# Kernel tuning notes

Measured on AMD Instinct MI355X. Metric: run time of the kernel, lower is better.

Reference implementation:

```python
import jax, jax.numpy as jnp
import numpy as np

IN_FEATURES = 2048
OUT_FEATURES = 2048
BATCH = 4096


def setup_inputs() -> dict:
    key = jax.random.key(0)
    k1, k2, k3, k4 = jax.random.split(key, 4)
    bound = 1.0 / (IN_FEATURES ** 0.5)
    x_re = jax.random.normal(k1, (BATCH, IN_FEATURES), dtype=jnp.float32)
    x_im = jax.random.normal(k2, (BATCH, IN_FEATURES), dtype=jnp.float32)
    # filters: (out_features, in_features), re/im each uniform(-bound, bound)
    w_re = jax.random.uniform(k3, (OUT_FEATURES, IN_FEATURES), dtype=jnp.float32, minval=-bound, maxval=bound)
    w_im = jax.random.uniform(k4, (OUT_FEATURES, IN_FEATURES), dtype=jnp.float32, minval=-bound, maxval=bound)
    return {"x_re": x_re, "x_im": x_im, "w_re": w_re, "w_im": w_im}


def reference(x_re, x_im, w_re, w_im):
    # Complex linear: (x_re + i x_im) @ (w_re + i w_im)^T, expressed as 4 real GEMMs.
    # Equivalent to torch: (inputs.unsqueeze(1) * filters).sum(-1) with complex64.
    out_re = jnp.einsum('bi,oi->bo', x_re, w_re) - jnp.einsum('bi,oi->bo', x_im, w_im)
    out_im = jnp.einsum('bi,oi->bo', x_re, w_im) + jnp.einsum('bi,oi->bo', x_im, w_re)
    # stack re/im -> (2, batch, out) to keep a single real-dtype output
    return jnp.stack([out_re, out_im], axis=0)
```

## Files before the change

kernel.cpp:

```cpp
#include <hip/hip_runtime.h>

typedef __bf16 bf16_t;
typedef __bf16 bf16x8 __attribute__((ext_vector_type(8)));
typedef __bf16 bf16x4 __attribute__((ext_vector_type(4)));
typedef float f32x4 __attribute__((ext_vector_type(4)));

#define M_DIM 4096
#define N_DIM 4096
#define K_DIM 4096
#define OUTF 2048
#define INF 2048
#define LDK 4096
#define NT 64

__global__ __launch_bounds__(256) void pack_ab(
    const float* __restrict__ xre, const float* __restrict__ xim,
    const float* __restrict__ wre, const float* __restrict__ wim,
    bf16_t* __restrict__ Abf, bf16_t* __restrict__ Bbf)
{
  size_t gid = (size_t)blockIdx.x * 256 + threadIdx.x;
  size_t e8  = gid * 8;
  const size_t MAT = (size_t)4096 * 4096;
  bool isB = e8 >= MAT;
  size_t e = isB ? (e8 - MAT) : e8;
  int row = (int)(e >> 12);
  int k   = (int)(e & 4095);

  const float* src;
  float s = 1.0f;
  if (!isB) {
    src = (k < INF) ? (xre + (size_t)row * INF + k)
                    : (xim + (size_t)row * INF + (k - INF));
  } else {
    if (row < OUTF) {
      if (k < INF) { src = wre + (size_t)row * INF + k; }
      else         { src = wim + (size_t)row * INF + (k - INF); s = -1.0f; }
    } else {
      int o = row - OUTF;
      src = (k < INF) ? (wim + (size_t)o * INF + k)
                      : (wre + (size_t)o * INF + (k - INF));
    }
  }
  const float4* p = reinterpret_cast<const float4*>(src);
  float4 f0 = p[0];
  float4 f1 = p[1];
  bf16x8 v;
  v[0] = (bf16_t)(f0.x * s); v[1] = (bf16_t)(f0.y * s);
  v[2] = (bf16_t)(f0.z * s); v[3] = (bf16_t)(f0.w * s);
  v[4] = (bf16_t)(f1.x * s); v[5] = (bf16_t)(f1.y * s);
  v[6] = (bf16_t)(f1.z * s); v[7] = (bf16_t)(f1.w * s);
  bf16_t* dst = (isB ? Bbf : Abf) + e;
  *reinterpret_cast<bf16x8*>(dst) = v;
}

__device__ __forceinline__ void gld_lds16(const void* g, void* l) {
  __builtin_amdgcn_global_load_lds(
      (const __attribute__((address_space(1))) void*)g,
      (__attribute__((address_space(3))) void*)l,
      16, 0, 0);
}


template<int QM, int QN>
__device__ __forceinline__ void mfma_quad(f32x4 (&acc)[8][4],
                                          const bf16x8 (&aF)[4][2],
                                          const bf16x8 (&bF)[2][2]) {
  __builtin_amdgcn_s_setprio(1);
#pragma unroll
  for (int m = 0; m < 4; ++m)
#pragma unroll
    for (int n = 0; n < 2; ++n) {
      f32x4 v = acc[QM * 4 + m][QN * 2 + n];
      v = __builtin_amdgcn_mfma_f32_16x16x32_bf16(aF[m][0], bF[n][0], v, 0, 0, 0);
      v = __builtin_amdgcn_mfma_f32_16x16x32_bf16(aF[m][1], bF[n][1], v, 0, 0, 0);
      acc[QM * 4 + m][QN * 2 + n] = v;
    }
  __builtin_amdgcn_s_setprio(0);
}

__global__ __launch_bounds__(512, 2) void gemm256(
    const bf16_t* __restrict__ A, const bf16_t* __restrict__ B,
    float* __restrict__ out)
{
  __shared__ alignas(16) bf16_t lds[2 * 32768];
  char* Lb = (char*)lds;

  const int tid  = threadIdx.x;
  const int lane = tid & 63;
  const int wid  = tid >> 6;
  const int wm   = wid >> 2;
  const int wn   = wid & 3;
  const int lr   = lane & 15;
  const int kg   = (lane >> 4) * 16;
  const int xm   = ((lr & 3) << 4) | (((lr >> 2) & 1) << 6);

  int bid = blockIdx.x;
  int swz = (bid & 7) * 32 + (bid >> 3);
  const int bm = swz >> 4;
  const int bn = swz & 15;

  int rS[2], kS[2];
#pragma unroll
  for (int j = 0; j < 2; ++j) {
    int P   = j * 8192 + tid * 16;
    int row = P >> 7;
    int p   = P & 127;
    int L   = p ^ ((row & 3) << 4) ^ (((row >> 2) & 1) << 6);
    rS[j] = row;
    kS[j] = L >> 1;
  }
  const bf16_t* As0 = A + (size_t)(bm * 256 + rS[0]) * LDK + kS[0];
  const bf16_t* As1 = A + (size_t)(bm * 256 + rS[1]) * LDK + kS[1];
  const bf16_t* Bs0 = B + (size_t)(bn * 256 + rS[0]) * LDK + kS[0];
  const bf16_t* Bs1 = B + (size_t)(bn * 256 + rS[1]) * LDK + kS[1];
  const int dst16 = tid * 16;

#define STAGE_A(t, h, c) do {                                                  \
    gld_lds16(As0 + (size_t)(h) * 128 * LDK + (t) * 64,                        \
              Lb + (c) * 65536 + (h) * 16384 + dst16);                         \
    gld_lds16(As1 + (size_t)(h) * 128 * LDK + (t) * 64,                        \
              Lb + (c) * 65536 + (h) * 16384 + 8192 + dst16);                  \
  } while (0)
#define STAGE_B(t, h, c) do {                                                  \
    gld_lds16(Bs0 + (size_t)(h) * 128 * LDK + (t) * 64,                        \
              Lb + (c) * 65536 + 32768 + (h) * 16384 + dst16);                 \
    gld_lds16(Bs1 + (size_t)(h) * 128 * LDK + (t) * 64,                        \
              Lb + (c) * 65536 + 32768 + (h) * 16384 + 8192 + dst16);          \
  } while (0)
#define RD_A(c, qm, m, ks)                                                     \
  (*(const bf16x8*)(Lb + (c) * 65536 + wm * 16384 +                            \
                    ((qm) * 64 + (m) * 16 + lr) * 128 +                        \
                    ((((ks) * 64) | kg) ^ xm)))
#define RD_B(c, qn, n, ks)                                                     \
  (*(const bf16x8*)(Lb + (c) * 65536 + 32768 + (wn >> 1) * 16384 +             \
                    ((wn & 1) * 64 + (qn) * 32 + (n) * 16 + lr) * 128 +        \
                    ((((ks) * 64) | kg) ^ xm)))
#define BAR()   __builtin_amdgcn_s_barrier()
#define SB()    __builtin_amdgcn_sched_barrier(0)
#define ISSUE_Q1(c) do {                                                       \
    _Pragma("unroll")                                                          \
    for (int m_ = 0; m_ < 4; ++m_) {                                           \
      a0[m_][0] = RD_A(c, 0, m_, 0);                                           \
      a0[m_][1] = RD_A(c, 0, m_, 1);                                           \
    }                                                                          \
    _Pragma("unroll")                                                          \
    for (int n_ = 0; n_ < 2; ++n_) {                                           \
      b0[n_][0] = RD_B(c, 0, n_, 0);                                           \
      b0[n_][1] = RD_B(c, 0, n_, 1);                                           \
    }                                                                          \
  } while (0)

  f32x4 acc[8][4];
#pragma unroll
  for (int i = 0; i < 8; ++i)
#pragma unroll
    for (int j = 0; j < 4; ++j)
      acc[i][j] = (f32x4){0.f, 0.f, 0.f, 0.f};

  bf16x8 a0[4][2], b0[2][2];

  STAGE_A(0, 0, 0); STAGE_A(0, 1, 0);
  STAGE_B(0, 0, 0); STAGE_B(0, 1, 0);
  STAGE_A(1, 0, 1);
  asm volatile("s_waitcnt vmcnt(2)" ::: "memory");
  BAR();
  ISSUE_Q1(0);
  SB();

  for (int t = 0; t < NT; ++t) {
    const int c = t & 1;
    bf16x8 a1[4][2], b1[2][2];

    if (t + 1 < NT) STAGE_A(t + 1, 1, c ^ 1);
#pragma unroll
    for (int n = 0; n < 2; ++n) {
      b1[n][0] = RD_B(c, 1, n, 0);
      b1[n][1] = RD_B(c, 1, n, 1);
    }
    SB();
    asm volatile("s_waitcnt lgkmcnt(4)" ::: "memory");
    SB();
    mfma_quad<0, 0>(acc, a0, b0);

    if (t + 1 < NT) STAGE_B(t + 1, 0, c ^ 1);
#pragma unroll
    for (int m = 0; m < 4; ++m) {
      a1[m][0] = RD_A(c, 1, m, 0);
      a1[m][1] = RD_A(c, 1, m, 1);
    }
    SB();
    asm volatile("s_waitcnt lgkmcnt(8)" ::: "memory");
    SB();
    mfma_quad<0, 1>(acc, a0, b1);

    if (t + 1 < NT) STAGE_B(t + 1, 1, c ^ 1);
    asm volatile("s_waitcnt lgkmcnt(0)" ::: "memory");
    SB();
    mfma_quad<1, 1>(acc, a1, b1);
    BAR();

    if (t + 2 < NT) STAGE_A(t + 2, 0, c);
    if (t + 2 < NT) {
      asm volatile("s_waitcnt vmcnt(2)" ::: "memory");
    } else if (t + 1 < NT) {
      asm volatile("s_waitcnt vmcnt(0)" ::: "memory");
    }
    BAR();
    mfma_quad<1, 0>(acc, a1, b0);
    if (t + 1 < NT) {
      SB();
      ISSUE_Q1(c ^ 1);
      SB();
    }
  }

  const size_t imOff = (size_t)M_DIM * OUTF;
  const int fq = (lane >> 4) * 4;
  const bool isIm = (bn * 256) >= OUTF;
  float* obase = out + (isIm ? imOff : 0);
  const int colBase = bn * 256 - (isIm ? OUTF : 0) + wn * 64;
#pragma unroll
  for (int ar = 0; ar < 8; ++ar) {
    int gr = bm * 256 + wm * 128 + ar * 16 + fq;
#pragma unroll
    for (int cc = 0; cc < 4; ++cc) {
      int gc = colBase + cc * 16 + lr;
#pragma unroll
      for (int j = 0; j < 4; ++j)
        obase[(size_t)(gr + j) * OUTF + gc] = acc[ar][cc][j];
    }
  }
#undef STAGE_A
#undef STAGE_B
#undef RD_A
#undef RD_B
#undef BAR
#undef SB
#undef ISSUE_Q1
}

__global__ __launch_bounds__(256) void gemm_fused(
    const float* __restrict__ xre, const float* __restrict__ xim,
    const float* __restrict__ wre, const float* __restrict__ wim,
    float* __restrict__ out)
{
  __shared__ alignas(16) bf16_t As[128 * 40];
  __shared__ alignas(16) bf16_t Bs[128 * 40];

  int tid = threadIdx.x;
  int bid = blockIdx.x;
  int swz = (bid & 7) * 128 + (bid >> 3);
  int bm = swz >> 5;
  int bn = swz & 31;

  int lane = tid & 63;
  int w    = tid >> 6;
  int wm   = (w >> 1) * 64;
  int wn   = (w & 1) * 64;
  int lr   = lane & 15;
  int lk   = (lane >> 4) * 8;

  f32x4 acc[4][4];
#pragma unroll
  for (int m = 0; m < 4; ++m)
#pragma unroll
    for (int n = 0; n < 4; ++n)
      acc[m][n] = (f32x4){0.f, 0.f, 0.f, 0.f};

  int srow = tid >> 3;
  int scol = (tid & 7) * 4;

  bool nIm  = (bn * 128) >= OUTF;
  int nbase = nIm ? (bn * 128 - OUTF) : (bn * 128);

  for (int kt = 0; kt < K_DIM / 32; ++kt) {
    int k0 = kt * 32;
    bool kHi = (k0 >= INF);
    int kk = kHi ? (k0 - INF) : k0;

    const float* Asrc = (kHi ? xim : xre) + (size_t)(bm * 128) * INF + kk;
    const float* Bsrc;
    float s = 1.0f;
    if (!nIm) { if (!kHi) { Bsrc = wre; } else { Bsrc = wim; s = -1.0f; } }
    else      { Bsrc = kHi ? wre : wim; }
    Bsrc += (size_t)nbase * INF + kk;

    float4 av[4], bv[4];
#pragma unroll
    for (int i = 0; i < 4; ++i) {
      av[i] = *reinterpret_cast<const float4*>(Asrc + (size_t)(srow + i * 32) * INF + scol);
      bv[i] = *reinterpret_cast<const float4*>(Bsrc + (size_t)(srow + i * 32) * INF + scol);
    }
    __syncthreads();
#pragma unroll
    for (int i = 0; i < 4; ++i) {
      bf16x4 a4, b4;
      a4[0] = (bf16_t)av[i].x; a4[1] = (bf16_t)av[i].y;
      a4[2] = (bf16_t)av[i].z; a4[3] = (bf16_t)av[i].w;
      b4[0] = (bf16_t)(bv[i].x * s); b4[1] = (bf16_t)(bv[i].y * s);
      b4[2] = (bf16_t)(bv[i].z * s); b4[3] = (bf16_t)(bv[i].w * s);
      *reinterpret_cast<bf16x4*>(&As[(srow + i * 32) * 40 + scol]) = a4;
      *reinterpret_cast<bf16x4*>(&Bs[(srow + i * 32) * 40 + scol]) = b4;
    }
    __syncthreads();

    bf16x8 a[4], b[4];
#pragma unroll
    for (int m = 0; m < 4; ++m)
      a[m] = *reinterpret_cast<const bf16x8*>(&As[(wm + m * 16 + lr) * 40 + lk]);
#pragma unroll
    for (int n = 0; n < 4; ++n)
      b[n] = *reinterpret_cast<const bf16x8*>(&Bs[(wn + n * 16 + lr) * 40 + lk]);
#pragma unroll
    for (int m = 0; m < 4; ++m)
#pragma unroll
      for (int n = 0; n < 4; ++n)
        acc[m][n] = __builtin_amdgcn_mfma_f32_16x16x32_bf16(a[m], b[n], acc[m][n], 0, 0, 0);
  }
  __syncthreads();

  const size_t imOff = (size_t)M_DIM * OUTF;
  int fq = (lane >> 4) * 4;
#pragma unroll
  for (int m = 0; m < 4; ++m) {
    int gr = bm * 128 + wm + m * 16 + fq;
#pragma unroll
    for (int n = 0; n < 4; ++n) {
      int gc = bn * 128 + wn + n * 16 + lr;
      float* dst = (gc < OUTF) ? (out + (size_t)gr * OUTF + gc)
                               : (out + imOff + (size_t)gr * OUTF + (gc - OUTF));
#pragma unroll
      for (int j = 0; j < 4; ++j)
        dst[(size_t)j * OUTF] = acc[m][n][j];
    }
  }
}

extern "C" void kernel_launch(void* const* d_in, const int* in_sizes, int n_in,
                              void* d_out, int out_size, void* d_ws, size_t ws_size,
                              hipStream_t stream) {
  const float* xre = (const float*)d_in[0];
  const float* xim = (const float*)d_in[1];
  const float* wre = (const float*)d_in[2];
  const float* wim = (const float*)d_in[3];
  float* out = (float*)d_out;

  const size_t need = (size_t)2 * 4096 * 4096 * sizeof(bf16_t);
  if (ws_size >= need) {
    bf16_t* Abf = (bf16_t*)d_ws;
    bf16_t* Bbf = Abf + (size_t)4096 * 4096;
    hipLaunchKernelGGL(pack_ab, dim3(16384), dim3(256), 0, stream,
                       xre, xim, wre, wim, Abf, Bbf);
    hipLaunchKernelGGL(gemm256, dim3(256), dim3(512), 0, stream,
                       Abf, Bbf, out);
  } else {
    hipLaunchKernelGGL(gemm_fused, dim3(1024), dim3(256), 0, stream,
                       xre, xim, wre, wim, out);
  }
}
```

Measured before the change: 141.9 us.

## Restructure GEMM main loop into barrier-synchronized 8-phase ping-pong schedule

Rewrites the bf16 MFMA main loop from a software-pipelined single-iteration body with sched_barriers and partial lgkmcnt waits into an explicitly unrolled two-tile loop. Each quadrant of MFMAs is bracketed by workgroup barriers and full LDS waits, and the global-to-LDS staging order changes so that B is prefetched before A. The aim is a ping-pong style schedule where waves alternate between memory and compute phases. In exchange it adds many more barriers per K-step and removes the overlap of LDS reads with the in-flight MFMAs, which could serialize work.

Result: slower. 145.2 us (+2.3%).

```diff
diff --git a/kernel.cpp b/kernel.cpp
--- a/kernel.cpp
+++ b/kernel.cpp
@@ -135,18 +135,29 @@
   (*(const bf16x8*)(Lb + (c) * 65536 + 32768 + (wn >> 1) * 16384 +             \
                     ((wn & 1) * 64 + (qn) * 32 + (n) * 16 + lr) * 128 +        \
                     ((((ks) * 64) | kg) ^ xm)))
-#define BAR()   __builtin_amdgcn_s_barrier()
-#define SB()    __builtin_amdgcn_sched_barrier(0)
-#define ISSUE_Q1(c) do {                                                       \
+#define BAR()     __builtin_amdgcn_s_barrier()
+#define LGKM(N)   asm volatile("s_waitcnt lgkmcnt(" #N ")" ::: "memory")
+#define VMC(N)    asm volatile("s_waitcnt vmcnt(" #N ")" ::: "memory")
+#define RD12(c) do {                                                           \
     _Pragma("unroll")                                                          \
     for (int m_ = 0; m_ < 4; ++m_) {                                           \
-      a0[m_][0] = RD_A(c, 0, m_, 0);                                           \
-      a0[m_][1] = RD_A(c, 0, m_, 1);                                           \
+      a0[m_][0] = RD_A(c, 0, m_, 0); a0[m_][1] = RD_A(c, 0, m_, 1);            \
     }                                                                          \
     _Pragma("unroll")                                                          \
     for (int n_ = 0; n_ < 2; ++n_) {                                           \
-      b0[n_][0] = RD_B(c, 0, n_, 0);                                           \
-      b0[n_][1] = RD_B(c, 0, n_, 1);                                           \
+      b0[n_][0] = RD_B(c, 0, n_, 0); b0[n_][1] = RD_B(c, 0, n_, 1);            \
+    }                                                                          \
+  } while (0)
+#define RD4(c) do {                                                            \
+    _Pragma("unroll")                                                          \
+    for (int n_ = 0; n_ < 2; ++n_) {                                           \
+      b1[n_][0] = RD_B(c, 1, n_, 0); b1[n_][1] = RD_B(c, 1, n_, 1);            \
+    }                                                                          \
+  } while (0)
+#define RD8(c) do {                                                            \
+    _Pragma("unroll")                                                          \
+    for (int m_ = 0; m_ < 4; ++m_) {                                           \
+      a1[m_][0] = RD_A(c, 1, m_, 0); a1[m_][1] = RD_A(c, 1, m_, 1);            \
     }                                                                          \
   } while (0)
 
@@ -157,61 +168,67 @@
     for (int j = 0; j < 4; ++j)
       acc[i][j] = (f32x4){0.f, 0.f, 0.f, 0.f};
 
-  bf16x8 a0[4][2], b0[2][2];
-
   STAGE_A(0, 0, 0); STAGE_A(0, 1, 0);
   STAGE_B(0, 0, 0); STAGE_B(0, 1, 0);
-  STAGE_A(1, 0, 1);
-  asm volatile("s_waitcnt vmcnt(2)" ::: "memory");
+  STAGE_B(1, 0, 1); STAGE_B(1, 1, 1);
+  VMC(4);
   BAR();
-  ISSUE_Q1(0);
-  SB();
-
-  for (int t = 0; t < NT; ++t) {
-    const int c = t & 1;
-    bf16x8 a1[4][2], b1[2][2];
-
-    if (t + 1 < NT) STAGE_A(t + 1, 1, c ^ 1);
-#pragma unroll
-    for (int n = 0; n < 2; ++n) {
-      b1[n][0] = RD_B(c, 1, n, 0);
-      b1[n][1] = RD_B(c, 1, n, 1);
-    }
-    SB();
-    asm volatile("s_waitcnt lgkmcnt(4)" ::: "memory");
-    SB();
+
+  for (int i = 0; i < NT / 2; ++i) {
+    const int u  = 2 * i;
+    const bool s2 = (u + 2 < NT);
+    const bool s3 = (u + 3 < NT);
+    bf16x8 a0[4][2], a1[4][2], b0[2][2], b1[2][2];
+
+    RD12(0);
+    STAGE_A(u + 1, 0, 1);
+    LGKM(8);
+    BAR(); LGKM(0);
     mfma_quad<0, 0>(acc, a0, b0);
-
-    if (t + 1 < NT) STAGE_B(t + 1, 0, c ^ 1);
-#pragma unroll
-    for (int m = 0; m < 4; ++m) {
-      a1[m][0] = RD_A(c, 1, m, 0);
-      a1[m][1] = RD_A(c, 1, m, 1);
-    }
-    SB();
-    asm volatile("s_waitcnt lgkmcnt(8)" ::: "memory");
-    SB();
+    BAR();
+
+    RD4(0);
+    STAGE_A(u + 1, 1, 1);
+    BAR(); LGKM(0);
     mfma_quad<0, 1>(acc, a0, b1);
-
-    if (t + 1 < NT) STAGE_B(t + 1, 1, c ^ 1);
-    asm volatile("s_waitcnt lgkmcnt(0)" ::: "memory");
-    SB();
+    BAR();
+
+    RD8(0);
+    if (s2) STAGE_B(u + 2, 0, 0);
+    BAR(); LGKM(0);
     mfma_quad<1, 1>(acc, a1, b1);
     BAR();
 
-    if (t + 2 < NT) STAGE_A(t + 2, 0, c);
-    if (t + 2 < NT) {
-      asm volatile("s_waitcnt vmcnt(2)" ::: "memory");
-    } else if (t + 1 < NT) {
-      asm volatile("s_waitcnt vmcnt(0)" ::: "memory");
-    }
+    if (s2) STAGE_B(u + 2, 1, 0);
     BAR();
     mfma_quad<1, 0>(acc, a1, b0);
-    if (t + 1 < NT) {
-      SB();
-      ISSUE_Q1(c ^ 1);
-      SB();
-    }
+    if (s2) { VMC(4); } else { VMC(0); }
+    BAR();
+
+    RD12(1);
+    if (s2) STAGE_A(u + 2, 0, 0);
+    LGKM(8);
+    BAR(); LGKM(0);
+    mfma_quad<0, 0>(acc, a0, b0);
+    BAR();
+
+    RD4(1);
+    if (s2) STAGE_A(u + 2, 1, 0);
+    BAR(); LGKM(0);
+    mfma_quad<0, 1>(acc, a0, b1);
+    BAR();
+
+    RD8(1);
+    if (s3) STAGE_B(u + 3, 0, 1);
+    BAR(); LGKM(0);
+    mfma_quad<1, 1>(acc, a1, b1);
+    BAR();
+
+    if (s3) STAGE_B(u + 3, 1, 1);
+    BAR();
+    mfma_quad<1, 0>(acc, a1, b0);
+    if (s3) { VMC(4); } else { VMC(0); }
+    BAR();
   }
 
   const size_t imOff = (size_t)M_DIM * OUTF;
@@ -235,8 +252,11 @@
 #undef RD_A
 #undef RD_B
 #undef BAR
-#undef SB
-#undef ISSUE_Q1
+#undef LGKM
+#undef VMC
+#undef RD12
+#undef RD4
+#undef RD8
 }
 
 __global__ __launch_bounds__(256) void gemm_fused(
```

## Use 3-multiplication complex GEMM (Gauss trick) with new pack and fused kernel

Applied to the files above, without the earlier changes.

Replaces the 4-real-GEMM formulation, packed as one 4096x4096x4096 GEMM, with the Gauss 3M trick. It packs (xr+xi), xi, xr and wr, -(wr+wi), wi-wr into bf16, then runs three K=2048 products, sharing accumulators so the real and imaginary outputs are built from three partial sums. This cuts MFMA work by a quarter but changes the tile to 256x128 with more barriers per k-tile, and adds extra rounding from bf16 sums of operands. The pack now reads and writes a somewhat different volume of data.

After: 164.0 us. 1.16x slower.

```diff
diff --git a/kernel.cpp b/kernel.cpp
--- a/kernel.cpp
+++ b/kernel.cpp
@@ -6,12 +6,236 @@
 typedef float f32x4 __attribute__((ext_vector_type(4)));
 
 #define M_DIM 4096
-#define N_DIM 4096
-#define K_DIM 4096
 #define OUTF 2048
 #define INF 2048
 #define LDK 4096
 #define NT 64
+#define LDK2 2048
+#define NT3 96
+
+__device__ __forceinline__ float mfq(float x) { return x; }
+
+__global__ __launch_bounds__(256) void pack_3m(
+    const float* __restrict__ xre, const float* __restrict__ xim,
+    const float* __restrict__ wre, const float* __restrict__ wim,
+    bf16_t* __restrict__ ws)
+{
+  size_t e = ((size_t)blockIdx.x * 256 + threadIdx.x) * 8;
+  const size_t AB = 25165824;
+  bf16x8 v;
+  if (e < AB) {
+    int seg = (int)(e / 8388608);
+    size_t off = e - (size_t)seg * 8388608;
+    size_t base = (off >> 11) * (size_t)INF + (off & 2047);
+    const float4* pr = reinterpret_cast<const float4*>(xre + base);
+    const float4* pi = reinterpret_cast<const float4*>(xim + base);
+#pragma unroll
+    for (int h = 0; h < 2; ++h) {
+      float4 fr = pr[h], fi = pi[h];
+      float r[4] = {fr.x, fr.y, fr.z, fr.w};
+      float ii[4] = {fi.x, fi.y, fi.z, fi.w};
+#pragma unroll
+      for (int j = 0; j < 4; ++j) {
+        float o = (seg == 0) ? (r[j] + ii[j]) : ((seg == 1) ? ii[j] : r[j]);
+        v[h * 4 + j] = (bf16_t)o;
+      }
+    }
+  } else {
+    size_t eb = e - AB;
+    int seg = (int)(eb / 4194304);
+    size_t off = eb - (size_t)seg * 4194304;
+    size_t base = (off >> 11) * (size_t)INF + (off & 2047);
+    const float4* pr = reinterpret_cast<const float4*>(wre + base);
+    const float4* pi = reinterpret_cast<const float4*>(wim + base);
+#pragma unroll
+    for (int h = 0; h < 2; ++h) {
+      float4 fr = pr[h], fi = pi[h];
+      float r[4] = {fr.x, fr.y, fr.z, fr.w};
+      float ii[4] = {fi.x, fi.y, fi.z, fi.w};
+#pragma unroll
+      for (int j = 0; j < 4; ++j) {
+        float o = (seg == 0) ? r[j] : ((seg == 1) ? -(r[j] + ii[j]) : (ii[j] - r[j]));
+        v[h * 4 + j] = (bf16_t)o;
+      }
+    }
+  }
+  *reinterpret_cast<bf16x8*>(ws + e) = v;
+}
+
+__device__ __forceinline__ void gld_lds16(const void* g, void* l) {
+  __builtin_amdgcn_global_load_lds(
+      (const __attribute__((address_space(1))) void*)g,
+      (__attribute__((address_space(3))) void*)l,
+      16, 0, 0);
+}
+
+__global__ __launch_bounds__(512, 2) void gemm3m(
+    const bf16_t* __restrict__ ws, float* __restrict__ out)
+{
+  __shared__ alignas(16) bf16_t lds[2 * 24576];
+  char* Lb = (char*)lds;
+
+  const int tid  = threadIdx.x;
+  const int lane = tid & 63;
+  const int wid  = tid >> 6;
+  const int wm2  = wid >> 1;
+  const int wn2  = wid & 1;
+  const int lr   = lane & 15;
+  const int kg   = (lane >> 4) * 16;
+  const int xm   = ((lr & 3) << 4) | (((lr >> 2) & 1) << 6);
+
+  int bid = blockIdx.x;
+  int swz = (bid & 7) * 32 + (bid >> 3);
+  const int bm = swz >> 4;
+  const int bn = swz & 15;
+
+  const int rowbase = tid >> 3;
+  const int pby     = (tid & 7) * 16;
+  const int Lg      = pby ^ ((rowbase & 3) << 4) ^ (((rowbase >> 2) & 1) << 6);
+  const int kelem   = Lg >> 1;
+  const int dst16   = tid * 16;
+
+  const bf16_t* Sb  = ws;
+  const bf16_t* XIb = ws + 8388608;
+  const bf16_t* XRb = ws + 16777216;
+  const bf16_t* B1b = ws + 25165824;
+  const bf16_t* B2b = ws + 29360128;
+  const bf16_t* B3b = ws + 33554432;
+
+  const size_t aoff = (size_t)(bm * 256 + rowbase) * LDK2 + kelem;
+  const size_t boff = (size_t)(bn * 128 + rowbase) * LDK2 + kelem;
+  const bf16_t* aB[3] = {Sb + aoff, XIb + aoff, XRb + aoff};
+  const bf16_t* bB[3] = {B1b + boff, B2b + boff, B3b + boff};
+
+#define STAGE_AH(u, h, c) do {                                                 \
+    int p_ = (u) >> 5, lt_ = (u) & 31;                                         \
+    const bf16_t* ab_ = aB[0];                                                 \
+    if (p_ == 1) ab_ = aB[1]; else if (p_ == 2) ab_ = aB[2];                   \
+    _Pragma("unroll")                                                          \
+    for (int j_ = 0; j_ < 2; ++j_)                                             \
+      gld_lds16(ab_ + (size_t)((h) * 128 + j_ * 64) * LDK2 + lt_ * 64,         \
+                Lb + (c) * 49152 + (h) * 16384 + j_ * 8192 + dst16);           \
+  } while (0)
+#define STAGE_B3(u, c) do {                                                    \
+    int p_ = (u) >> 5, lt_ = (u) & 31;                                         \
+    const bf16_t* bb_ = bB[0];                                                 \
+    if (p_ == 1) bb_ = bB[1]; else if (p_ == 2) bb_ = bB[2];                   \
+    _Pragma("unroll")                                                          \
+    for (int j_ = 0; j_ < 2; ++j_)                                             \
+      gld_lds16(bb_ + (size_t)(j_ * 64) * LDK2 + lt_ * 64,                     \
+                Lb + (c) * 49152 + 32768 + j_ * 8192 + dst16);                 \
+  } while (0)
+#define RD_A3(c, h, m_, ks)                                                    \
+  (*(const bf16x8*)(Lb + (c) * 49152 +                                         \
+      (wm2 * 64 + (h) * 32 + (m_) * 16 + lr) * 128 + ((((ks) * 64) | kg) ^ xm)))
+#define RD_B3(c, g, n_, ks)                                                    \
+  (*(const bf16x8*)(Lb + (c) * 49152 + 32768 +                                 \
+      (wn2 * 64 + (g) * 32 + (n_) * 16 + lr) * 128 + ((((ks) * 64) | kg) ^ xm)))
+#define BAR()   __builtin_amdgcn_s_barrier()
+#define LGKM0() asm volatile("s_waitcnt lgkmcnt(0)" ::: "memory")
+#define MQ(ACC, h, g, AF, BF) do {                                             \
+    __builtin_amdgcn_s_setprio(1);                                             \
+    _Pragma("unroll")                                                          \
+    for (int m_ = 0; m_ < 2; ++m_)                                             \
+    _Pragma("unroll")                                                          \
+    for (int n_ = 0; n_ < 2; ++n_) {                                           \
+      f32x4 v_ = ACC[(h) * 2 + m_][(g) * 2 + n_];                              \
+      v_ = __builtin_amdgcn_mfma_f32_16x16x32_bf16(AF[m_][0], BF[n_][0], v_,   \
+                                                   0, 0, 0);                   \
+      v_ = __builtin_amdgcn_mfma_f32_16x16x32_bf16(AF[m_][1], BF[n_][1], v_,   \
+                                                   0, 0, 0);                   \
+      ACC[(h) * 2 + m_][(g) * 2 + n_] = v_;                                    \
+    }                                                                          \
+    __builtin_amdgcn_s_setprio(0);                                             \
+  } while (0)
+#define KTILE(u, ACC) do {                                                     \
+    const int c_ = (u) & 1;                                                    \
+    bf16x8 a0[2][2], a1[2][2], b0[2][2], b1[2][2];                             \
+    _Pragma("unroll")                                                          \
+    for (int m_ = 0; m_ < 2; ++m_) {                                           \
+      a0[m_][0] = RD_A3(c_, 0, m_, 0); a0[m_][1] = RD_A3(c_, 0, m_, 1);        \
+    }                                                                          \
+    _Pragma("unroll")                                                          \
+    for (int n_ = 0; n_ < 2; ++n_) {                                           \
+      b0[n_][0] = RD_B3(c_, 0, n_, 0); b0[n_][1] = RD_B3(c_, 0, n_, 1);        \
+    }                                                                          \
+    if ((u) + 1 < NT3) STAGE_AH((u) + 1, 1, c_ ^ 1);                           \
+    BAR(); LGKM0();                                                            \
+    MQ(ACC, 0, 0, a0, b0);                                                     \
+    BAR();                                                                     \
+    _Pragma("unroll")                                                          \
+    for (int n_ = 0; n_ < 2; ++n_) {                                           \
+      b1[n_][0] = RD_B3(c_, 1, n_, 0); b1[n_][1] = RD_B3(c_, 1, n_, 1);        \
+    }                                                                          \
+    if ((u) + 1 < NT3) STAGE_B3((u) + 1, c_ ^ 1);                              \
+    BAR(); LGKM0();                                                            \
+    MQ(ACC, 0, 1, a0, b1);                                                     \
+    BAR();                                                                     \
+    _Pragma("unroll")                                                          \
+    for (int m_ = 0; m_ < 2; ++m_) {                                           \
+      a1[m_][0] = RD_A3(c_, 1, m_, 0); a1[m_][1] = RD_A3(c_, 1, m_, 1);        \
+    }                                                                          \
+    BAR(); LGKM0();                                                            \
+    MQ(ACC, 1, 1, a1, b1);                                                     \
+    BAR();                                                                     \
+    if ((u) + 2 < NT3) STAGE_AH((u) + 2, 0, c_);                               \
+    MQ(ACC, 1, 0, a1, b0);                                                     \
+    if ((u) + 2 < NT3) {                                                       \
+      asm volatile("s_waitcnt vmcnt(2)" ::: "memory");                         \
+    } else if ((u) + 1 < NT3) {                                                \
+      asm volatile("s_waitcnt vmcnt(0)" ::: "memory");                         \
+    }                                                                          \
+    BAR();                                                                     \
+  } while (0)
+
+  f32x4 accR[4][4], accI[4][4];
+#pragma unroll
+  for (int i = 0; i < 4; ++i)
+#pragma unroll
+    for (int j = 0; j < 4; ++j)
+      accR[i][j] = (f32x4){0.f, 0.f, 0.f, 0.f};
+
+  STAGE_AH(0, 0, 0); STAGE_AH(0, 1, 0);
+  STAGE_B3(0, 0);
+  STAGE_AH(1, 0, 1);
+  asm volatile("s_waitcnt vmcnt(2)" ::: "memory");
+  BAR();
+
+  for (int t = 0; t < 32; ++t) KTILE(t, accR);
+
+#pragma unroll
+  for (int i = 0; i < 4; ++i)
+#pragma unroll
+    for (int j = 0; j < 4; ++j)
+      accI[i][j] = accR[i][j];
+
+  for (int t = 32; t < 64; ++t) KTILE(t, accR);
+  for (int t = 64; t < 96; ++t) KTILE(t, accI);
+
+  const size_t imOff = (size_t)M_DIM * OUTF;
+  const int fq = (lane >> 4) * 4;
+#pragma unroll
+  for (int Mt = 0; Mt < 4; ++Mt) {
+    int gr = bm * 256 + wm2 * 64 + Mt * 16 + fq;
+#pragma unroll
+    for (int Nt = 0; Nt < 4; ++Nt) {
+      int gc = bn * 128 + wn2 * 64 + Nt * 16 + lr;
+#pragma unroll
+      for (int j = 0; j < 4; ++j) {
+        out[(size_t)(gr + j) * OUTF + gc]         = accR[Mt][Nt][j];
+        out[imOff + (size_t)(gr + j) * OUTF + gc] = accI[Mt][Nt][j];
+      }
+    }
+  }
+#undef STAGE_AH
+#undef STAGE_B3
+#undef RD_A3
+#undef RD_B3
+#undef BAR
+#undef LGKM0
+#undef MQ
+#undef KTILE
+}
 
 __global__ __launch_bounds__(256) void pack_ab(
     const float* __restrict__ xre, const float* __restrict__ xim,
@@ -25,7 +249,6 @@
   size_t e = isB ? (e8 - MAT) : e8;
   int row = (int)(e >> 12);
   int k   = (int)(e & 4095);
-
   const float* src;
   float s = 1.0f;
   if (!isB) {
@@ -53,14 +276,6 @@
   *reinterpret_cast<bf16x8*>(dst) = v;
 }
 
-__device__ __forceinline__ void gld_lds16(const void* g, void* l) {
-  __builtin_amdgcn_global_load_lds(
-      (const __attribute__((address_space(1))) void*)g,
-      (__attribute__((address_space(3))) void*)l,
-      16, 0, 0);
-}
-
-
 template<int QM, int QN>
 __device__ __forceinline__ void mfma_quad(f32x4 (&acc)[8][4],
                                           const bf16x8 (&aF)[4][2],
@@ -84,7 +299,6 @@
 {
   __shared__ alignas(16) bf16_t lds[2 * 32768];
   char* Lb = (char*)lds;
-
   const int tid  = threadIdx.x;
   const int lane = tid & 63;
   const int wid  = tid >> 6;
@@ -93,12 +307,10 @@
   const int lr   = lane & 15;
   const int kg   = (lane >> 4) * 16;
   const int xm   = ((lr & 3) << 4) | (((lr >> 2) & 1) << 6);
-
   int bid = blockIdx.x;
   int swz = (bid & 7) * 32 + (bid >> 3);
   const int bm = swz >> 4;
   const int bn = swz & 15;
-
   int rS[2], kS[2];
 #pragma unroll
   for (int j = 0; j < 2; ++j) {
@@ -114,7 +326,6 @@
   const bf16_t* Bs0 = B + (size_t)(bn * 256 + rS[0]) * LDK + kS[0];
   const bf16_t* Bs1 = B + (size_t)(bn * 256 + rS[1]) * LDK + kS[1];
   const int dst16 = tid * 16;
-
 #define STAGE_A(t, h, c) do {                                                  \
     gld_lds16(As0 + (size_t)(h) * 128 * LDK + (t) * 64,                        \
               Lb + (c) * 65536 + (h) * 16384 + dst16);                         \
@@ -149,16 +360,13 @@
       b0[n_][1] = RD_B(c, 0, n_, 1);                                           \
     }                                                                          \
   } while (0)
-
   f32x4 acc[8][4];
 #pragma unroll
   for (int i = 0; i < 8; ++i)
 #pragma unroll
     for (int j = 0; j < 4; ++j)
       acc[i][j] = (f32x4){0.f, 0.f, 0.f, 0.f};
-
   bf16x8 a0[4][2], b0[2][2];
-
   STAGE_A(0, 0, 0); STAGE_A(0, 1, 0);
   STAGE_B(0, 0, 0); STAGE_B(0, 1, 0);
   STAGE_A(1, 0, 1);
@@ -166,11 +374,9 @@
   BAR();
   ISSUE_Q1(0);
   SB();
-
   for (int t = 0; t < NT; ++t) {
     const int c = t & 1;
     bf16x8 a1[4][2], b1[2][2];
-
     if (t + 1 < NT) STAGE_A(t + 1, 1, c ^ 1);
 #pragma unroll
     for (int n = 0; n < 2; ++n) {
@@ -181,7 +387,6 @@
     asm volatile("s_waitcnt lgkmcnt(4)" ::: "memory");
     SB();
     mfma_quad<0, 0>(acc, a0, b0);
-
     if (t + 1 < NT) STAGE_B(t + 1, 0, c ^ 1);
 #pragma unroll
     for (int m = 0; m < 4; ++m) {
@@ -192,13 +397,11 @@
     asm volatile("s_waitcnt lgkmcnt(8)" ::: "memory");
     SB();
     mfma_quad<0, 1>(acc, a0, b1);
-
     if (t + 1 < NT) STAGE_B(t + 1, 1, c ^ 1);
     asm volatile("s_waitcnt lgkmcnt(0)" ::: "memory");
     SB();
     mfma_quad<1, 1>(acc, a1, b1);
     BAR();
-
     if (t + 2 < NT) STAGE_A(t + 2, 0, c);
     if (t + 2 < NT) {
       asm volatile("s_waitcnt vmcnt(2)" ::: "memory");
@@ -213,7 +416,6 @@
       SB();
     }
   }
-
   const size_t imOff = (size_t)M_DIM * OUTF;
   const int fq = (lane >> 4) * 4;
   const bool isIm = (bn * 256) >= OUTF;
@@ -246,45 +448,37 @@
 {
   __shared__ alignas(16) bf16_t As[128 * 40];
   __shared__ alignas(16) bf16_t Bs[128 * 40];
-
   int tid = threadIdx.x;
   int bid = blockIdx.x;
   int swz = (bid & 7) * 128 + (bid >> 3);
   int bm = swz >> 5;
   int bn = swz & 31;
-
   int lane = tid & 63;
   int w    = tid >> 6;
   int wm   = (w >> 1) * 64;
   int wn   = (w & 1) * 64;
   int lr   = lane & 15;
   int lk   = (lane >> 4) * 8;
-
   f32x4 acc[4][4];
 #pragma unroll
   for (int m = 0; m < 4; ++m)
 #pragma unroll
     for (int n = 0; n < 4; ++n)
       acc[m][n] = (f32x4){0.f, 0.f, 0.f, 0.f};
-
   int srow = tid >> 3;
   int scol = (tid & 7) * 4;
-
   bool nIm  = (bn * 128) >= OUTF;
   int nbase = nIm ? (bn * 128 - OUTF) : (bn * 128);
-
-  for (int kt = 0; kt < K_DIM / 32; ++kt) {
+  for (int kt = 0; kt < (2 * INF) / 32; ++kt) {
     int k0 = kt * 32;
     bool kHi = (k0 >= INF);
     int kk = kHi ? (k0 - INF) : k0;
-
     const float* Asrc = (kHi ? xim : xre) + (size_t)(bm * 128) * INF + kk;
     const float* Bsrc;
     float s = 1.0f;
     if (!nIm) { if (!kHi) { Bsrc = wre; } else { Bsrc = wim; s = -1.0f; } }
     else      { Bsrc = kHi ? wre : wim; }
     Bsrc += (size_t)nbase * INF + kk;
-
     float4 av[4], bv[4];
 #pragma unroll
     for (int i = 0; i < 4; ++i) {
@@ -303,7 +497,6 @@
       *reinterpret_cast<bf16x4*>(&Bs[(srow + i * 32) * 40 + scol]) = b4;
     }
     __syncthreads();
-
     bf16x8 a[4], b[4];
 #pragma unroll
     for (int m = 0; m < 4; ++m)
@@ -318,7 +511,6 @@
         acc[m][n] = __builtin_amdgcn_mfma_f32_16x16x32_bf16(a[m], b[n], acc[m][n], 0, 0, 0);
   }
   __syncthreads();
-
   const size_t imOff = (size_t)M_DIM * OUTF;
   int fq = (lane >> 4) * 4;
 #pragma unroll
@@ -345,8 +537,14 @@
   const float* wim = (const float*)d_in[3];
   float* out = (float*)d_out;
 
-  const size_t need = (size_t)2 * 4096 * 4096 * sizeof(bf16_t);
-  if (ws_size >= need) {
+  const size_t need3m = (size_t)37748736 * sizeof(bf16_t);
+  const size_t need2  = (size_t)2 * 4096 * 4096 * sizeof(bf16_t);
+  if (ws_size >= need3m) {
+    bf16_t* wsb = (bf16_t*)d_ws;
+    hipLaunchKernelGGL(pack_3m, dim3(18432), dim3(256), 0, stream,
+                       xre, xim, wre, wim, wsb);
+    hipLaunchKernelGGL(gemm3m, dim3(256), dim3(512), 0, stream, wsb, out);
+  } else if (ws_size >= need2) {
     bf16_t* Abf = (bf16_t*)d_ws;
     bf16_t* Bbf = Abf + (size_t)4096 * 4096;
     hipLaunchKernelGGL(pack_ab, dim3(16384), dim3(256), 0, stream,
```
